# Performance work log

Hardware: AMD Instinct MI355X
Metric: run time of the kernel (lower is better)

Reference implementation:

```python
import jax, jax.numpy as jnp
import numpy as np

SMOOTH = 1.0
MAX_DIST = 10


def _neighbor_conv(x):
    # 3x3 ones kernel with zero center, padding=1 (NCHW, C=1)
    k = jnp.ones((1, 1, 3, 3), x.dtype).at[0, 0, 1, 1].set(0.0)
    return jax.lax.conv_general_dilated(
        x, k, window_strides=(1, 1), padding=[(1, 1), (1, 1)],
        dimension_numbers=('NCHW', 'OIHW', 'NCHW'))


def _analyze_skeleton(skel):
    n = _neighbor_conv(skel)
    on = skel > 0.5
    endpoints = ((n == 1) & on).astype(skel.dtype)
    midpoints = ((n == 2) & on).astype(skel.dtype)
    junctions = ((n > 2) & on).astype(skel.dtype)
    return endpoints, midpoints, junctions


def _iou(p, g):
    inter = jnp.sum(p * g, axis=(2, 3))
    union = jnp.sum(p, axis=(2, 3)) + jnp.sum(g, axis=(2, 3)) - inter
    return (inter + SMOOTH) / (union + SMOOTH)


def _structural_similarity(pred_skel, gt_skel):
    pe, pm, pj = _analyze_skeleton(pred_skel)
    ge, gm, gj = _analyze_skeleton(gt_skel)
    e_iou, m_iou, j_iou = _iou(pe, ge), _iou(pm, gm), _iou(pj, gj)
    ge_c = jnp.sum(ge, axis=(2, 3))
    gj_c = jnp.sum(gj, axis=(2, 3))
    gm_c = jnp.sum(gm, axis=(2, 3))
    total = ge_c + gj_c + gm_c + SMOOTH
    loss = 1.0 - ((ge_c / total) * e_iou + (gj_c / total) * j_iou + (gm_c / total) * m_iou)
    return loss.mean()


def _maxpool3(x):
    return jax.lax.reduce_window(
        x, -jnp.inf, jax.lax.max,
        window_dimensions=(1, 1, 3, 3), window_strides=(1, 1, 1, 1),
        padding=[(0, 0), (0, 0), (1, 1), (1, 1)])


def _distance_approximation(target, reference):
    # Fixed MAX_DIST iterations; identical math to the torch early-exit loop
    # because new_points requires ~found_mask (no distance is overwritten).
    tgt_on = target > 0.5

    def step(carry, d):
        dilated, found, dist = carry
        dilated = _maxpool3(dilated)
        new = (dilated > 0.5) & tgt_on & (~found)
        dist = dist + d.astype(dist.dtype) * new.astype(dist.dtype)
        return (dilated, found | new, dist), None

    init = (reference, jnp.zeros(target.shape, bool), jnp.zeros_like(target))
    (_, found, dist), _ = jax.lax.scan(step, init, jnp.arange(1, MAX_DIST + 1, dtype=jnp.int32))
    unfound = tgt_on & (~found)
    dist = dist + jnp.asarray(MAX_DIST, dist.dtype) * unfound.astype(dist.dtype)
    total_points = jnp.sum(tgt_on.astype(dist.dtype), axis=(2, 3))
    return jnp.sum(dist, axis=(2, 3)) / (total_points + SMOOTH)


def _medial_axis_distance(pred_skel, gt_skel):
    p2g = _distance_approximation(pred_skel, gt_skel)
    g2p = _distance_approximation(gt_skel, pred_skel)
    return (((p2g + g2p) / 2.0) / MAX_DIST).mean()


def setup_inputs() -> dict:
    key = jax.random.key(0)
    k1, k2 = jax.random.split(key)
    B, C, H, W = 32, 1, 512, 512
    pred_skel = jax.random.uniform(k1, (B, C, H, W), dtype=jnp.float32)
    gt_skel = (jax.random.uniform(k2, (B, C, H, W), dtype=jnp.float32) < 0.1).astype(jnp.float32)
    return {"pred_skel": pred_skel, "gt_skel": gt_skel}


def reference(pred_skel, gt_skel):
    inter = jnp.sum(pred_skel * gt_skel, axis=(2, 3))
    psum = jnp.sum(pred_skel, axis=(2, 3))
    gsum = jnp.sum(gt_skel, axis=(2, 3))
    dice = (2.0 * inter + SMOOTH) / (psum + gsum + SMOOTH)
    dice_loss = 1.0 - dice.mean()
    structural_loss = _structural_similarity(pred_skel, gt_skel)
    medial_loss = _medial_axis_distance(pred_skel, gt_skel)
    avg_mag = (dice_loss + structural_loss + medial_loss) / 3.0
    bal_dice = dice_loss / (dice_loss + SMOOTH) * avg_mag
    bal_struct = structural_loss / (structural_loss + SMOOTH) * avg_mag
    bal_medial = medial_loss / (medial_loss + SMOOTH) * avg_mag
    return bal_dice + bal_struct + bal_medial
```

## Files before the change

### kernel.cpp

```cpp
#include <hip/hip_runtime.h>
#include <stdint.h>

#define BATCH 32
#define H 512
#define W 512
#define NACC 16
#define TH 32
#define HALO 9
#define RH (TH + 2*HALO)
#define NWORDS (RH*8)
#define NT 1024
#define NW (NT/64)
#define NTILE (H/TH)
#define NBLK (NTILE*BATCH)


__global__ __launch_bounds__(NT, 4) void fused_kernel(
    const float* __restrict__ pred, const float* __restrict__ gt,
    float* __restrict__ part)
{
    __shared__ uint64_t MpS[NWORDS + 2];
    __shared__ uint64_t MgS[NWORDS + 2];
    __shared__ uint64_t Ge[TH * 8];
    __shared__ uint64_t Gm[TH * 8];
    __shared__ uint64_t Gj[TH * 8];
    __shared__ float    EC[2][TH];
    __shared__ float    redf[NW][2];
    __shared__ unsigned redu[NW][3];

    uint64_t* Mp = MpS + 1;
    uint64_t* Mg = MgS + 1;

    int fid  = blockIdx.x;
    int b    = fid & 31;
    int tile = fid >> 5;

    const float* pimg = pred + (size_t)b * H * W;
    const float* gimg = gt   + (size_t)b * H * W;
    int y0 = tile * TH;
    int tid = threadIdx.x, lane = tid & 63, wid = tid >> 6;

    float v0 = 0.f, v1 = 0.f;
    for (int s0 = wid; s0 < NWORDS; s0 += 4 * NW) {
        float vp[4], vg[4];
        #pragma unroll
        for (int u = 0; u < 4; ++u) {
            int s = s0 + u * NW;
            vp[u] = 0.f; vg[u] = 0.f;
            int ry = y0 - HALO + (s >> 3);
            if (s < NWORDS && (unsigned)ry < (unsigned)H) {
                int i0 = ry * W + (s & 7) * 64 + lane;
                vp[u] = pimg[i0]; vg[u] = gimg[i0];
            }
        }
        #pragma unroll
        for (int u = 0; u < 4; ++u) {
            int s = s0 + u * NW;
            if (s < NWORDS) {
                unsigned long long mp = __ballot(vp[u] > 0.5f);
                unsigned long long mg = __ballot(vg[u] > 0.5f);
                if (lane == 0) { Mp[s] = mp; Mg[s] = mg; }
                int r = s >> 3;
                if (r >= HALO && r < HALO + TH) {
                    v1 += vp[u];
                    v0 += (vg[u] > 0.5f) ? vp[u] : 0.f;
                }
            }
        }
    }
    if (tid == 0) { MpS[0] = 0; MpS[NWORDS + 1] = 0; MgS[0] = 0; MgS[NWORDS + 1] = 0; }

    bool isStencil = tid >= 512;
    int idx = tid & 511;
    int qi = idx & 127, h2 = idx >> 7;
    int x4 = qi * 4;
    int ys = y0 + h2 * 8;
    float4 pm4 = make_float4(0, 0, 0, 0), pc4 = make_float4(0, 0, 0, 0);
    if (isStencil) {
        if (ys > 0) pm4 = *(const float4*)(pimg + (size_t)(ys - 1) * W + x4);
        pc4 = *(const float4*)(pimg + (size_t)ys * W + x4);
    }

    if (tid < 2 * TH) {
        int c = tid >> 5, r = tid & (TH - 1);
        int y = y0 + r, col = 255 + c;
        float sum = (y > 0     ? pimg[(size_t)(y - 1) * W + col] : 0.f)
                  +              pimg[(size_t)y * W + col]
                  + (y < H - 1 ? pimg[(size_t)(y + 1) * W + col] : 0.f);
        EC[c][r] = sum;
    }
    __syncthreads();

    unsigned cge = 0, cgm = 0, cgj = 0;
    if (tid < 256) {
        int r = tid >> 3, w = tid & 7;
        int oM = (HALO + r) * 8 + w;
        bool wl = (w > 0), wr = (w < 7);
        uint64_t A  = Mg[oM - 8], Bm = Mg[oM], Cm = Mg[oM + 8];
        uint64_t AL = wl ? Mg[oM - 9] : 0ULL, AR = wr ? Mg[oM - 7] : 0ULL;
        uint64_t BL = wl ? Mg[oM - 1] : 0ULL, BR = wr ? Mg[oM + 1] : 0ULL;
        uint64_t CL = wl ? Mg[oM + 7] : 0ULL, CR = wr ? Mg[oM + 9] : 0ULL;
        uint64_t Aw = (A  << 1) | (AL >> 63), Ae = (A  >> 1) | (AR << 63);
        uint64_t Bw = (Bm << 1) | (BL >> 63), Be = (Bm >> 1) | (BR << 63);
        uint64_t Cw = (Cm << 1) | (CL >> 63), Ce = (Cm >> 1) | (CR << 63);
        uint64_t c1, c2, c3, c5;
        uint64_t t;
        t = Aw ^ A;  uint64_t s1 = t ^ Ae;  c1 = (Aw & A)  | (Ae & t);
        t = Bw ^ Be; uint64_t s2 = t ^ Cw;  c2 = (Bw & Be) | (Cw & t);
        t = Cm ^ Ce; uint64_t s3 = t ^ s1;  c3 = (Cm & Ce) | (s1 & t);
        uint64_t b0 = s2 ^ s3, c4 = s2 & s3;
        t = c1 ^ c2; uint64_t s5 = t ^ c3;  c5 = (c1 & c2) | (c3 & t);
        uint64_t b1 = s5 ^ c4, c6 = s5 & c4;
        uint64_t b2 = c5 ^ c6, b3 = c5 & c6;
        uint64_t nz23 = ~(b2 | b3);
        uint64_t ge = Bm & b0 & ~b1 & nz23;
        uint64_t gm = Bm & b1 & ~b0 & nz23;
        uint64_t gj = Bm & (b2 | b3 | (b1 & b0));
        Ge[tid] = ge; Gm[tid] = gm; Gj[tid] = gj;
        cge = (unsigned)__popcll(ge);
        cgm = (unsigned)__popcll(gm);
        cgj = (unsigned)__popcll(gj);
    }
    __syncthreads();

    uint64_t cpack = 0ULL;
    int dsum = 0, dcnt = 0;

    if (isStencil) {
        int wdx = qi >> 4;
        int ss = (qi & 15) * 4;

        for (int r = 0; r < 8; ++r) {
            int y = ys + r;
            float4 pp4 = (y < H - 1) ? *(const float4*)(pimg + (size_t)(y + 1) * W + x4)
                                     : make_float4(0, 0, 0, 0);
            int ry = h2 * 8 + r;
            uint64_t gew = Ge[ry * 8 + wdx];
            uint64_t gmw = Gm[ry * 8 + wdx];
            uint64_t gjw = Gj[ry * 8 + wdx];

            float ps[6];
            ps[1] = pm4.x + pc4.x + pp4.x; ps[2] = pm4.y + pc4.y + pp4.y;
            ps[3] = pm4.z + pc4.z + pp4.z; ps[4] = pm4.w + pc4.w + pp4.w;
            float psl = __shfl_up(ps[4], 1, 64);
            float psr = __shfl_down(ps[1], 1, 64);
            if (lane == 0)  psl = (qi == 0)   ? 0.f : EC[0][ry];
            if (lane == 63) psr = (qi == 127) ? 0.f : EC[1][ry];
            ps[0] = psl; ps[5] = psr;

            float pcv[4] = {pc4.x, pc4.y, pc4.z, pc4.w};
            #pragma unroll
            for (int j = 0; j < 4; ++j) {
                float np = ps[j] + ps[j + 1] + ps[j + 2] - pcv[j];
                bool pon = pcv[j] > 0.5f;
                bool pe  = pon && (np == 1.f);
                bool pmb = pon && (np == 2.f);
                bool pjb = pon && (np > 2.f);
                unsigned geb = (unsigned)(gew >> (ss + j)) & 1u;
                unsigned gmb = (unsigned)(gmw >> (ss + j)) & 1u;
                unsigned gjb = (unsigned)(gjw >> (ss + j)) & 1u;
                cpack += (uint64_t)pe
                       | ((uint64_t)pmb << 7)
                       | ((uint64_t)pjb << 14)
                       | ((uint64_t)(pe  && geb) << 21)
                       | ((uint64_t)(pmb && gmb) << 28)
                       | ((uint64_t)(pjb && gjb) << 35);
            }
            pm4 = pc4; pc4 = pp4;
        }
    } else {
        bool isP = tid < 256;
        int di = tid & 255;
        int o  = (HALO + (di >> 3)) * 8 + (di & 7);
        int w  = di & 7;
        bool wL = (w > 0), wR = (w < 7);
        const uint64_t* MT = isP ? Mp : Mg;
        const uint64_t* MV = isP ? Mg : Mp;

        uint64_t T = MT[o];
        dcnt = __popcll(T);
        dsum = dcnt;
        uint64_t VM = MV[o];
        uint64_t VL = wL ? MV[o - 1] : 0ULL;
        uint64_t VR = wR ? MV[o + 1] : 0ULL;
        uint64_t C = VM;

        #pragma unroll
        for (int a = 1; a <= 9; ++a) {
            int lo = o - 8 * a, hi = o + 8 * a;
            uint64_t NM = MV[lo] | MV[hi];
            uint64_t NL = wL ? (MV[lo - 1] | MV[hi - 1]) : 0ULL;
            uint64_t NR = wR ? (MV[lo + 1] | MV[hi + 1]) : 0ULL;
            uint64_t SL = NL, SM = NM, SR = NR;
            const int m = a - 1;
            if (m >= 1) {
                SM |= (SM << 1) | (SM >> 1) | (SL >> 63) | (SR << 63);
                SL |= SL << 1; SR |= SR >> 1;
            }
            if (m >= 2) {
                const int s = (m == 2) ? 1 : 2;
                SM |= (SM << s) | (SM >> s) | (SL >> (64 - s)) | (SR << (64 - s));
                SL |= SL << s; SR |= SR >> s;
            }
            if (m >= 4) {
                const int s = (m - 3 < 4) ? (m - 3) : 4;
                SM |= (SM << s) | (SM >> s) | (SL >> (64 - s)) | (SR << (64 - s));
                SL |= SL << s; SR |= SR >> s;
            }
            if (m >= 8) {
                const int s = m - 7;
                SM |= (SM << s) | (SM >> s) | (SL >> (64 - s)) | (SR << (64 - s));
                SL |= SL << s; SR |= SR >> s;
            }
            C |= SM;
            VL |= NL; VM |= NM; VR |= NR;
            C |= (VM << a) | (VM >> a) | (VL >> (64 - a)) | (VR << (64 - a));
            uint64_t rem = T & ~C;
            dsum += __popcll(rem);
            if (__all(rem == 0ULL)) break;
        }
    }

    unsigned r0, r1, r2;
    if (isStencil) {
        unsigned c_pe = (unsigned)( cpack        & 0x7F);
        unsigned c_pm = (unsigned)((cpack >> 7 ) & 0x7F);
        unsigned c_pj = (unsigned)((cpack >> 14) & 0x7F);
        unsigned c_ie = (unsigned)((cpack >> 21) & 0x7F);
        unsigned c_im = (unsigned)((cpack >> 28) & 0x7F);
        unsigned c_ij = (unsigned)((cpack >> 35) & 0x7F);
        r0 = c_pe | (c_pm << 16); r1 = c_pj | (c_ie << 16); r2 = c_im | (c_ij << 16);
    } else {
        r0 = (unsigned)dsum | ((unsigned)dcnt << 16);
        r1 = cge | (cgm << 16);
        r2 = cgj;
    }
    #pragma unroll
    for (int off = 32; off; off >>= 1) {
        v0 += __shfl_down(v0, off, 64);
        v1 += __shfl_down(v1, off, 64);
        r0 += __shfl_down(r0, off, 64);
        r1 += __shfl_down(r1, off, 64);
        r2 += __shfl_down(r2, off, 64);
    }
    if (lane == 0) {
        redf[wid][0] = v0; redf[wid][1] = v1;
        redu[wid][0] = r0; redu[wid][1] = r1; redu[wid][2] = r2;
    }
    __syncthreads();
    if (tid < 16) {
        int k = tid;
        float s = 0.f;
        if (k < 2) {
            #pragma unroll
            for (int wv = 0; wv < NW; ++wv) s += redf[wv][k];
        } else {
            static const uint8_t WB[16] = {0,0, 4, 8,8,8, 0,0,0, 8,8,8, 0,0,4,4};
            static const uint8_t WC[16] = {0,0, 4, 8,8,8, 4,4,4, 8,8,8, 4,4,4,4};
            static const uint8_t RG[16] = {0,0, 0, 0,0,1, 1,1,2, 1,2,2, 0,0,0,0};
            static const uint8_t HI[16] = {0,0, 1, 0,1,0, 0,1,0, 1,0,1, 0,1,0,1};
            unsigned u = 0;
            for (int wv = WB[k]; wv < WB[k] + WC[k]; ++wv)
                u += (redu[wv][RG[k]] >> (HI[k] * 16)) & 0xFFFFu;
            s = (float)u;
        }
        part[fid * NACC + k] = s;
    }
}

__global__ __launch_bounds__(512) void final_kernel(
    const float* __restrict__ part, float* __restrict__ out)
{
    __shared__ float sacc[BATCH][NACC];
    __shared__ float tri[BATCH][3];
    int t = threadIdx.x;
    {
        int b = t >> 4, k = t & 15;
        float s = 0.f;
        #pragma unroll 4
        for (int j = 0; j < NTILE; ++j)
            s += part[((j << 5) + b) * NACC + k];
        sacc[b][k] = s;
    }
    __syncthreads();
    if (t < BATCH) {
        const float* a = sacc[t];
        float inter = a[0], psum = a[1], gsum = a[2];
        float dice = (2.f * inter + 1.f) / (psum + gsum + 1.f);

        float pe = a[3], pm = a[4], pj = a[5];
        float ge = a[6], gm = a[7], gj = a[8];
        float ie = a[9], im = a[10], ij = a[11];
        float e_iou = (ie + 1.f) / (pe + ge - ie + 1.f);
        float m_iou = (im + 1.f) / (pm + gm - im + 1.f);
        float j_iou = (ij + 1.f) / (pj + gj - ij + 1.f);
        float total = ge + gj + gm + 1.f;
        float sloss = 1.f - ((ge / total) * e_iou + (gj / total) * j_iou + (gm / total) * m_iou);

        float p2g = a[12] / (a[13] + 1.f);
        float g2p = a[14] / (a[15] + 1.f);
        float med = ((p2g + g2p) * 0.5f) / 10.f;
        tri[t][0] = dice; tri[t][1] = sloss; tri[t][2] = med;
    }
    __syncthreads();
    if (t == 0) {
        float dice = 0.f, sloss = 0.f, med = 0.f;
        for (int b = 0; b < BATCH; ++b) {
            dice += tri[b][0]; sloss += tri[b][1]; med += tri[b][2];
        }
        float dice_loss  = 1.f - dice / (float)BATCH;
        float structural = sloss / (float)BATCH;
        float medial     = med / (float)BATCH;
        float avg = (dice_loss + structural + medial) / 3.f;
        float r = dice_loss  / (dice_loss  + 1.f) * avg
                + structural / (structural + 1.f) * avg
                + medial     / (medial     + 1.f) * avg;
        out[0] = r;
    }
}

extern "C" void kernel_launch(void* const* d_in, const int* in_sizes, int n_in,
                              void* d_out, int out_size, void* d_ws, size_t ws_size,
                              hipStream_t stream)
{
    const float* pred = (const float*)d_in[0];
    const float* gt   = (const float*)d_in[1];
    float* part = (float*)d_ws;
    float* out  = (float*)d_out;

    fused_kernel<<<dim3(NBLK), NT, 0, stream>>>(pred, gt, part);
    final_kernel<<<1, 512, 0, stream>>>(part, out);
}
```

Baseline: 112.0 us.

## Spread stencil and distance search across all threads with 32-bit words

The old kernel split work by thread role: 512 threads ran the float stencil over 8 rows each while 512 ran the distance search on 64-bit mask words. Now all 1024 threads run the stencil over 4 rows each, and all 1024 run the distance search on 32-bit half-words, which halves per-thread shift/popcount width. The aim is to balance the two phases and remove idle divergence between role groups. In exchange the reduction needs more shuffle channels and a reworked lookup table, and the 32-bit search uses twice as many neighbour-word loads.

```diff
diff --git a/kernel.cpp b/kernel.cpp
--- a/kernel.cpp
+++ b/kernel.cpp
@@ -26,7 +26,7 @@
     __shared__ uint64_t Gj[TH * 8];
     __shared__ float    EC[2][TH];
     __shared__ float    redf[NW][2];
-    __shared__ unsigned redu[NW][3];
+    __shared__ unsigned redu[NW][6];
 
     uint64_t* Mp = MpS + 1;
     uint64_t* Mg = MgS + 1;
@@ -70,16 +70,12 @@
     }
     if (tid == 0) { MpS[0] = 0; MpS[NWORDS + 1] = 0; MgS[0] = 0; MgS[NWORDS + 1] = 0; }
 
-    bool isStencil = tid >= 512;
-    int idx = tid & 511;
-    int qi = idx & 127, h2 = idx >> 7;
+    int qi = tid & 127, band = tid >> 7;
     int x4 = qi * 4;
-    int ys = y0 + h2 * 8;
-    float4 pm4 = make_float4(0, 0, 0, 0), pc4 = make_float4(0, 0, 0, 0);
-    if (isStencil) {
-        if (ys > 0) pm4 = *(const float4*)(pimg + (size_t)(ys - 1) * W + x4);
-        pc4 = *(const float4*)(pimg + (size_t)ys * W + x4);
-    }
+    int ys = y0 + band * 4;
+    float4 pm4 = make_float4(0, 0, 0, 0), pc4;
+    if (ys > 0) pm4 = *(const float4*)(pimg + (size_t)(ys - 1) * W + x4);
+    pc4 = *(const float4*)(pimg + (size_t)ys * W + x4);
 
     if (tid < 2 * TH) {
         int c = tid >> 5, r = tid & (TH - 1);
@@ -103,8 +99,7 @@
         uint64_t Aw = (A  << 1) | (AL >> 63), Ae = (A  >> 1) | (AR << 63);
         uint64_t Bw = (Bm << 1) | (BL >> 63), Be = (Bm >> 1) | (BR << 63);
         uint64_t Cw = (Cm << 1) | (CL >> 63), Ce = (Cm >> 1) | (CR << 63);
-        uint64_t c1, c2, c3, c5;
-        uint64_t t;
+        uint64_t c1, c2, c3, c5, t;
         t = Aw ^ A;  uint64_t s1 = t ^ Ae;  c1 = (Aw & A)  | (Ae & t);
         t = Bw ^ Be; uint64_t s2 = t ^ Cw;  c2 = (Bw & Be) | (Cw & t);
         t = Cm ^ Ce; uint64_t s3 = t ^ s1;  c3 = (Cm & Ce) | (s1 & t);
@@ -121,20 +116,73 @@
         cgm = (unsigned)__popcll(gm);
         cgj = (unsigned)__popcll(gj);
     }
+
+    int dsum = 0, dcnt = 0;
+    {
+        const uint32_t* Mp32 = (const uint32_t*)Mp;
+        const uint32_t* Mg32 = (const uint32_t*)Mg;
+        bool isP = tid < 512;
+        int di = tid & 511;
+        int o  = (HALO + (di >> 4)) * 16 + (di & 15);
+        int h  = di & 15;
+        bool wL = (h > 0), wR = (h < 15);
+        const uint32_t* MT = isP ? Mp32 : Mg32;
+        const uint32_t* MV = isP ? Mg32 : Mp32;
+
+        uint32_t T = MT[o];
+        dcnt = __popc(T);
+        dsum = dcnt;
+        uint32_t VM = MV[o];
+        uint32_t VL = wL ? MV[o - 1] : 0u;
+        uint32_t VR = wR ? MV[o + 1] : 0u;
+        uint32_t C = VM;
+
+        #pragma unroll
+        for (int a = 1; a <= 9; ++a) {
+            int lo = o - 16 * a, hi = o + 16 * a;
+            uint32_t NM = MV[lo] | MV[hi];
+            uint32_t NL = wL ? (MV[lo - 1] | MV[hi - 1]) : 0u;
+            uint32_t NR = wR ? (MV[lo + 1] | MV[hi + 1]) : 0u;
+            uint32_t SL = NL, SM = NM, SR = NR;
+            const int m = a - 1;
+            if (m >= 1) {
+                SM |= (SM << 1) | (SM >> 1) | (SL >> 31) | (SR << 31);
+                SL |= SL << 1; SR |= SR >> 1;
+            }
+            if (m >= 2) {
+                const int s = (m == 2) ? 1 : 2;
+                SM |= (SM << s) | (SM >> s) | (SL >> (32 - s)) | (SR << (32 - s));
+                SL |= SL << s; SR |= SR >> s;
+            }
+            if (m >= 4) {
+                const int s = (m - 3 < 4) ? (m - 3) : 4;
+                SM |= (SM << s) | (SM >> s) | (SL >> (32 - s)) | (SR << (32 - s));
+                SL |= SL << s; SR |= SR >> s;
+            }
+            if (m >= 8) {
+                const int s = m - 7;
+                SM |= (SM << s) | (SM >> s) | (SL >> (32 - s)) | (SR << (32 - s));
+                SL |= SL << s; SR |= SR >> s;
+            }
+            C |= SM;
+            VL |= NL; VM |= NM; VR |= NR;
+            C |= (VM << a) | (VM >> a) | (VL >> (32 - a)) | (VR << (32 - a));
+            uint32_t rem = T & ~C;
+            dsum += __popc(rem);
+            if (__all(rem == 0u)) break;
+        }
+    }
     __syncthreads();
 
     uint64_t cpack = 0ULL;
-    int dsum = 0, dcnt = 0;
-
-    if (isStencil) {
+    {
         int wdx = qi >> 4;
         int ss = (qi & 15) * 4;
-
-        for (int r = 0; r < 8; ++r) {
+        for (int r = 0; r < 4; ++r) {
             int y = ys + r;
             float4 pp4 = (y < H - 1) ? *(const float4*)(pimg + (size_t)(y + 1) * W + x4)
                                      : make_float4(0, 0, 0, 0);
-            int ry = h2 * 8 + r;
+            int ry = band * 4 + r;
             uint64_t gew = Ge[ry * 8 + wdx];
             uint64_t gmw = Gm[ry * 8 + wdx];
             uint64_t gjw = Gj[ry * 8 + wdx];
@@ -168,73 +216,20 @@
             }
             pm4 = pc4; pc4 = pp4;
         }
-    } else {
-        bool isP = tid < 256;
-        int di = tid & 255;
-        int o  = (HALO + (di >> 3)) * 8 + (di & 7);
-        int w  = di & 7;
-        bool wL = (w > 0), wR = (w < 7);
-        const uint64_t* MT = isP ? Mp : Mg;
-        const uint64_t* MV = isP ? Mg : Mp;
-
-        uint64_t T = MT[o];
-        dcnt = __popcll(T);
-        dsum = dcnt;
-        uint64_t VM = MV[o];
-        uint64_t VL = wL ? MV[o - 1] : 0ULL;
-        uint64_t VR = wR ? MV[o + 1] : 0ULL;
-        uint64_t C = VM;
-
-        #pragma unroll
-        for (int a = 1; a <= 9; ++a) {
-            int lo = o - 8 * a, hi = o + 8 * a;
-            uint64_t NM = MV[lo] | MV[hi];
-            uint64_t NL = wL ? (MV[lo - 1] | MV[hi - 1]) : 0ULL;
-            uint64_t NR = wR ? (MV[lo + 1] | MV[hi + 1]) : 0ULL;
-            uint64_t SL = NL, SM = NM, SR = NR;
-            const int m = a - 1;
-            if (m >= 1) {
-                SM |= (SM << 1) | (SM >> 1) | (SL >> 63) | (SR << 63);
-                SL |= SL << 1; SR |= SR >> 1;
-            }
-            if (m >= 2) {
-                const int s = (m == 2) ? 1 : 2;
-                SM |= (SM << s) | (SM >> s) | (SL >> (64 - s)) | (SR << (64 - s));
-                SL |= SL << s; SR |= SR >> s;
-            }
-            if (m >= 4) {
-                const int s = (m - 3 < 4) ? (m - 3) : 4;
-                SM |= (SM << s) | (SM >> s) | (SL >> (64 - s)) | (SR << (64 - s));
-                SL |= SL << s; SR |= SR >> s;
-            }
-            if (m >= 8) {
-                const int s = m - 7;
-                SM |= (SM << s) | (SM >> s) | (SL >> (64 - s)) | (SR << (64 - s));
-                SL |= SL << s; SR |= SR >> s;
-            }
-            C |= SM;
-            VL |= NL; VM |= NM; VR |= NR;
-            C |= (VM << a) | (VM >> a) | (VL >> (64 - a)) | (VR << (64 - a));
-            uint64_t rem = T & ~C;
-            dsum += __popcll(rem);
-            if (__all(rem == 0ULL)) break;
-        }
-    }
-
-    unsigned r0, r1, r2;
-    if (isStencil) {
-        unsigned c_pe = (unsigned)( cpack        & 0x7F);
-        unsigned c_pm = (unsigned)((cpack >> 7 ) & 0x7F);
-        unsigned c_pj = (unsigned)((cpack >> 14) & 0x7F);
-        unsigned c_ie = (unsigned)((cpack >> 21) & 0x7F);
-        unsigned c_im = (unsigned)((cpack >> 28) & 0x7F);
-        unsigned c_ij = (unsigned)((cpack >> 35) & 0x7F);
-        r0 = c_pe | (c_pm << 16); r1 = c_pj | (c_ie << 16); r2 = c_im | (c_ij << 16);
-    } else {
-        r0 = (unsigned)dsum | ((unsigned)dcnt << 16);
-        r1 = cge | (cgm << 16);
-        r2 = cgj;
-    }
+    }
+
+    unsigned c_pe = (unsigned)( cpack        & 0x7F);
+    unsigned c_pm = (unsigned)((cpack >> 7 ) & 0x7F);
+    unsigned c_pj = (unsigned)((cpack >> 14) & 0x7F);
+    unsigned c_ie = (unsigned)((cpack >> 21) & 0x7F);
+    unsigned c_im = (unsigned)((cpack >> 28) & 0x7F);
+    unsigned c_ij = (unsigned)((cpack >> 35) & 0x7F);
+    unsigned r0 = (unsigned)dsum | ((unsigned)dcnt << 16);
+    unsigned r1 = c_pe | (c_pm << 16);
+    unsigned r2 = c_pj | (c_ie << 16);
+    unsigned r3 = c_im | (c_ij << 16);
+    unsigned r4 = cge | (cgm << 16);
+    unsigned r5 = cgj;
     #pragma unroll
     for (int off = 32; off; off >>= 1) {
         v0 += __shfl_down(v0, off, 64);
@@ -242,10 +237,14 @@
         r0 += __shfl_down(r0, off, 64);
         r1 += __shfl_down(r1, off, 64);
         r2 += __shfl_down(r2, off, 64);
+        r3 += __shfl_down(r3, off, 64);
+        r4 += __shfl_down(r4, off, 64);
+        r5 += __shfl_down(r5, off, 64);
     }
     if (lane == 0) {
         redf[wid][0] = v0; redf[wid][1] = v1;
         redu[wid][0] = r0; redu[wid][1] = r1; redu[wid][2] = r2;
+        redu[wid][3] = r3; redu[wid][4] = r4; redu[wid][5] = r5;
     }
     __syncthreads();
     if (tid < 16) {
@@ -255,10 +254,10 @@
             #pragma unroll
             for (int wv = 0; wv < NW; ++wv) s += redf[wv][k];
         } else {
-            static const uint8_t WB[16] = {0,0, 4, 8,8,8, 0,0,0, 8,8,8, 0,0,4,4};
-            static const uint8_t WC[16] = {0,0, 4, 8,8,8, 4,4,4, 8,8,8, 4,4,4,4};
-            static const uint8_t RG[16] = {0,0, 0, 0,0,1, 1,1,2, 1,2,2, 0,0,0,0};
-            static const uint8_t HI[16] = {0,0, 1, 0,1,0, 0,1,0, 1,0,1, 0,1,0,1};
+            static const uint8_t WB[16] = {0,0, 8, 0,0,0,  0,0,0, 0,0,0,   0,0,8,8};
+            static const uint8_t WC[16] = {0,0, 8, 16,16,16, 4,4,4, 16,16,16, 8,8,8,8};
+            static const uint8_t RG[16] = {0,0, 0, 1,1,2,  4,4,5, 2,3,3,   0,0,0,0};
+            static const uint8_t HI[16] = {0,0, 1, 0,1,0,  0,1,0, 1,0,1,   0,1,0,1};
             unsigned u = 0;
             for (int wv = WB[k]; wv < WB[k] + WC[k]; ++wv)
                 u += (redu[wv][RG[k]] >> (HI[k] * 16)) & 0xFFFFu;
```

Result: no change. 111.6 us (-0.4%).

## Halve block size and run distance and stencil phases sequentially per thread

Applied to the files above, without the earlier changes.

The block shrinks from 1024 to 512 threads. Instead of splitting the threads into separate stencil and distance-search groups, every thread now runs the bitmask distance search and then the 8-row stencil pass. The reduction carries six packed counters and two float accumulator pairs, and the lookup tables are remapped to match. This targets idle time from the imbalance between the two groups and may allow more resident blocks, but it lengthens each thread's serial path and raises register pressure.

```diff
diff --git a/kernel.cpp b/kernel.cpp
--- a/kernel.cpp
+++ b/kernel.cpp
@@ -9,8 +9,8 @@
 #define HALO 9
 #define RH (TH + 2*HALO)
 #define NWORDS (RH*8)
-#define NT 1024
-#define NW (NT/64)
+#define NT 512
+#define NW 8
 #define NTILE (H/TH)
 #define NBLK (NTILE*BATCH)
 
@@ -25,8 +25,8 @@
     __shared__ uint64_t Gm[TH * 8];
     __shared__ uint64_t Gj[TH * 8];
     __shared__ float    EC[2][TH];
-    __shared__ float    redf[NW][2];
-    __shared__ unsigned redu[NW][3];
+    __shared__ float    redf[16][2];
+    __shared__ unsigned redu[NW][6];
 
     uint64_t* Mp = MpS + 1;
     uint64_t* Mg = MgS + 1;
@@ -40,7 +40,7 @@
     int y0 = tile * TH;
     int tid = threadIdx.x, lane = tid & 63, wid = tid >> 6;
 
-    float v0 = 0.f, v1 = 0.f;
+    float v0A = 0.f, v1A = 0.f, v0B = 0.f, v1B = 0.f;
     for (int s0 = wid; s0 < NWORDS; s0 += 4 * NW) {
         float vp[4], vg[4];
         #pragma unroll
@@ -62,24 +62,25 @@
                 if (lane == 0) { Mp[s] = mp; Mg[s] = mg; }
                 int r = s >> 3;
                 if (r >= HALO && r < HALO + TH) {
-                    v1 += vp[u];
-                    v0 += (vg[u] > 0.5f) ? vp[u] : 0.f;
+                    if ((u & 1) == 0) {
+                        v1A += vp[u];
+                        v0A += (vg[u] > 0.5f) ? vp[u] : 0.f;
+                    } else {
+                        v1B += vp[u];
+                        v0B += (vg[u] > 0.5f) ? vp[u] : 0.f;
+                    }
                 }
             }
         }
     }
     if (tid == 0) { MpS[0] = 0; MpS[NWORDS + 1] = 0; MgS[0] = 0; MgS[NWORDS + 1] = 0; }
 
-    bool isStencil = tid >= 512;
-    int idx = tid & 511;
-    int qi = idx & 127, h2 = idx >> 7;
+    int qi = tid & 127, h2 = tid >> 7;
     int x4 = qi * 4;
     int ys = y0 + h2 * 8;
-    float4 pm4 = make_float4(0, 0, 0, 0), pc4 = make_float4(0, 0, 0, 0);
-    if (isStencil) {
-        if (ys > 0) pm4 = *(const float4*)(pimg + (size_t)(ys - 1) * W + x4);
-        pc4 = *(const float4*)(pimg + (size_t)ys * W + x4);
-    }
+    float4 pm4 = make_float4(0, 0, 0, 0), pc4;
+    if (ys > 0) pm4 = *(const float4*)(pimg + (size_t)(ys - 1) * W + x4);
+    pc4 = *(const float4*)(pimg + (size_t)ys * W + x4);
 
     if (tid < 2 * TH) {
         int c = tid >> 5, r = tid & (TH - 1);
@@ -93,8 +94,8 @@
 
     unsigned cge = 0, cgm = 0, cgj = 0;
     if (tid < 256) {
-        int r = tid >> 3, w = tid & 7;
-        int oM = (HALO + r) * 8 + w;
+        int rr = tid >> 3, w = tid & 7;
+        int oM = (HALO + rr) * 8 + w;
         bool wl = (w > 0), wr = (w < 7);
         uint64_t A  = Mg[oM - 8], Bm = Mg[oM], Cm = Mg[oM + 8];
         uint64_t AL = wl ? Mg[oM - 9] : 0ULL, AR = wr ? Mg[oM - 7] : 0ULL;
@@ -103,8 +104,7 @@
         uint64_t Aw = (A  << 1) | (AL >> 63), Ae = (A  >> 1) | (AR << 63);
         uint64_t Bw = (Bm << 1) | (BL >> 63), Be = (Bm >> 1) | (BR << 63);
         uint64_t Cw = (Cm << 1) | (CL >> 63), Ce = (Cm >> 1) | (CR << 63);
-        uint64_t c1, c2, c3, c5;
-        uint64_t t;
+        uint64_t c1, c2, c3, c5, t;
         t = Aw ^ A;  uint64_t s1 = t ^ Ae;  c1 = (Aw & A)  | (Ae & t);
         t = Bw ^ Be; uint64_t s2 = t ^ Cw;  c2 = (Bw & Be) | (Cw & t);
         t = Cm ^ Ce; uint64_t s3 = t ^ s1;  c3 = (Cm & Ce) | (s1 & t);
@@ -121,15 +121,66 @@
         cgm = (unsigned)__popcll(gm);
         cgj = (unsigned)__popcll(gj);
     }
+
+    int dsum = 0, dcnt = 0;
+    {
+        bool isP = tid < 256;
+        int di = tid & 255;
+        int o  = (HALO + (di >> 3)) * 8 + (di & 7);
+        int w  = di & 7;
+        bool wL = (w > 0), wR = (w < 7);
+        const uint64_t* MT = isP ? Mp : Mg;
+        const uint64_t* MV = isP ? Mg : Mp;
+
+        uint64_t T = MT[o];
+        dcnt = __popcll(T);
+        dsum = dcnt;
+        uint64_t VM = MV[o];
+        uint64_t VL = wL ? MV[o - 1] : 0ULL;
+        uint64_t VR = wR ? MV[o + 1] : 0ULL;
+        uint64_t C = VM;
+
+        #pragma unroll
+        for (int a = 1; a <= 9; ++a) {
+            int lo = o - 8 * a, hi = o + 8 * a;
+            uint64_t NM = MV[lo] | MV[hi];
+            uint64_t NL = wL ? (MV[lo - 1] | MV[hi - 1]) : 0ULL;
+            uint64_t NR = wR ? (MV[lo + 1] | MV[hi + 1]) : 0ULL;
+            uint64_t SL = NL, SM = NM, SR = NR;
+            const int m = a - 1;
+            if (m >= 1) {
+                SM |= (SM << 1) | (SM >> 1) | (SL >> 63) | (SR << 63);
+                SL |= SL << 1; SR |= SR >> 1;
+            }
+            if (m >= 2) {
+                const int s = (m == 2) ? 1 : 2;
+                SM |= (SM << s) | (SM >> s) | (SL >> (64 - s)) | (SR << (64 - s));
+                SL |= SL << s; SR |= SR >> s;
+            }
+            if (m >= 4) {
+                const int s = (m - 3 < 4) ? (m - 3) : 4;
+                SM |= (SM << s) | (SM >> s) | (SL >> (64 - s)) | (SR << (64 - s));
+                SL |= SL << s; SR |= SR >> s;
+            }
+            if (m >= 8) {
+                const int s = m - 7;
+                SM |= (SM << s) | (SM >> s) | (SL >> (64 - s)) | (SR << (64 - s));
+                SL |= SL << s; SR |= SR >> s;
+            }
+            C |= SM;
+            VL |= NL; VM |= NM; VR |= NR;
+            C |= (VM << a) | (VM >> a) | (VL >> (64 - a)) | (VR << (64 - a));
+            uint64_t rem = T & ~C;
+            dsum += __popcll(rem);
+            if (__all(rem == 0ULL)) break;
+        }
+    }
     __syncthreads();
 
     uint64_t cpack = 0ULL;
-    int dsum = 0, dcnt = 0;
-
-    if (isStencil) {
+    {
         int wdx = qi >> 4;
         int ss = (qi & 15) * 4;
-
         for (int r = 0; r < 8; ++r) {
             int y = ys + r;
             float4 pp4 = (y < H - 1) ? *(const float4*)(pimg + (size_t)(y + 1) * W + x4)
@@ -168,84 +219,38 @@
             }
             pm4 = pc4; pc4 = pp4;
         }
-    } else {
-        bool isP = tid < 256;
-        int di = tid & 255;
-        int o  = (HALO + (di >> 3)) * 8 + (di & 7);
-        int w  = di & 7;
-        bool wL = (w > 0), wR = (w < 7);
-        const uint64_t* MT = isP ? Mp : Mg;
-        const uint64_t* MV = isP ? Mg : Mp;
-
-        uint64_t T = MT[o];
-        dcnt = __popcll(T);
-        dsum = dcnt;
-        uint64_t VM = MV[o];
-        uint64_t VL = wL ? MV[o - 1] : 0ULL;
-        uint64_t VR = wR ? MV[o + 1] : 0ULL;
-        uint64_t C = VM;
-
-        #pragma unroll
-        for (int a = 1; a <= 9; ++a) {
-            int lo = o - 8 * a, hi = o + 8 * a;
-            uint64_t NM = MV[lo] | MV[hi];
-            uint64_t NL = wL ? (MV[lo - 1] | MV[hi - 1]) : 0ULL;
-            uint64_t NR = wR ? (MV[lo + 1] | MV[hi + 1]) : 0ULL;
-            uint64_t SL = NL, SM = NM, SR = NR;
-            const int m = a - 1;
-            if (m >= 1) {
-                SM |= (SM << 1) | (SM >> 1) | (SL >> 63) | (SR << 63);
-                SL |= SL << 1; SR |= SR >> 1;
-            }
-            if (m >= 2) {
-                const int s = (m == 2) ? 1 : 2;
-                SM |= (SM << s) | (SM >> s) | (SL >> (64 - s)) | (SR << (64 - s));
-                SL |= SL << s; SR |= SR >> s;
-            }
-            if (m >= 4) {
-                const int s = (m - 3 < 4) ? (m - 3) : 4;
-                SM |= (SM << s) | (SM >> s) | (SL >> (64 - s)) | (SR << (64 - s));
-                SL |= SL << s; SR |= SR >> s;
-            }
-            if (m >= 8) {
-                const int s = m - 7;
-                SM |= (SM << s) | (SM >> s) | (SL >> (64 - s)) | (SR << (64 - s));
-                SL |= SL << s; SR |= SR >> s;
-            }
-            C |= SM;
-            VL |= NL; VM |= NM; VR |= NR;
-            C |= (VM << a) | (VM >> a) | (VL >> (64 - a)) | (VR << (64 - a));
-            uint64_t rem = T & ~C;
-            dsum += __popcll(rem);
-            if (__all(rem == 0ULL)) break;
-        }
-    }
-
-    unsigned r0, r1, r2;
-    if (isStencil) {
-        unsigned c_pe = (unsigned)( cpack        & 0x7F);
-        unsigned c_pm = (unsigned)((cpack >> 7 ) & 0x7F);
-        unsigned c_pj = (unsigned)((cpack >> 14) & 0x7F);
-        unsigned c_ie = (unsigned)((cpack >> 21) & 0x7F);
-        unsigned c_im = (unsigned)((cpack >> 28) & 0x7F);
-        unsigned c_ij = (unsigned)((cpack >> 35) & 0x7F);
-        r0 = c_pe | (c_pm << 16); r1 = c_pj | (c_ie << 16); r2 = c_im | (c_ij << 16);
-    } else {
-        r0 = (unsigned)dsum | ((unsigned)dcnt << 16);
-        r1 = cge | (cgm << 16);
-        r2 = cgj;
-    }
+    }
+
+    unsigned c_pe = (unsigned)( cpack        & 0x7F);
+    unsigned c_pm = (unsigned)((cpack >> 7 ) & 0x7F);
+    unsigned c_pj = (unsigned)((cpack >> 14) & 0x7F);
+    unsigned c_ie = (unsigned)((cpack >> 21) & 0x7F);
+    unsigned c_im = (unsigned)((cpack >> 28) & 0x7F);
+    unsigned c_ij = (unsigned)((cpack >> 35) & 0x7F);
+    unsigned r0 = (unsigned)dsum | ((unsigned)dcnt << 16);
+    unsigned r1 = c_pe | (c_pm << 16);
+    unsigned r2 = c_pj | (c_ie << 16);
+    unsigned r3 = c_im | (c_ij << 16);
+    unsigned r4 = cge | (cgm << 16);
+    unsigned r5 = cgj;
     #pragma unroll
     for (int off = 32; off; off >>= 1) {
-        v0 += __shfl_down(v0, off, 64);
-        v1 += __shfl_down(v1, off, 64);
+        v0A += __shfl_down(v0A, off, 64);
+        v1A += __shfl_down(v1A, off, 64);
+        v0B += __shfl_down(v0B, off, 64);
+        v1B += __shfl_down(v1B, off, 64);
         r0 += __shfl_down(r0, off, 64);
         r1 += __shfl_down(r1, off, 64);
         r2 += __shfl_down(r2, off, 64);
+        r3 += __shfl_down(r3, off, 64);
+        r4 += __shfl_down(r4, off, 64);
+        r5 += __shfl_down(r5, off, 64);
     }
     if (lane == 0) {
-        redf[wid][0] = v0; redf[wid][1] = v1;
+        redf[wid][0] = v0A;     redf[wid][1] = v1A;
+        redf[wid + 8][0] = v0B; redf[wid + 8][1] = v1B;
         redu[wid][0] = r0; redu[wid][1] = r1; redu[wid][2] = r2;
+        redu[wid][3] = r3; redu[wid][4] = r4; redu[wid][5] = r5;
     }
     __syncthreads();
     if (tid < 16) {
@@ -253,11 +258,11 @@
         float s = 0.f;
         if (k < 2) {
             #pragma unroll
-            for (int wv = 0; wv < NW; ++wv) s += redf[wv][k];
+            for (int wv = 0; wv < 16; ++wv) s += redf[wv][k];
         } else {
-            static const uint8_t WB[16] = {0,0, 4, 8,8,8, 0,0,0, 8,8,8, 0,0,4,4};
+            static const uint8_t WB[16] = {0,0, 4, 0,0,0, 0,0,0, 0,0,0, 0,0,4,4};
             static const uint8_t WC[16] = {0,0, 4, 8,8,8, 4,4,4, 8,8,8, 4,4,4,4};
-            static const uint8_t RG[16] = {0,0, 0, 0,0,1, 1,1,2, 1,2,2, 0,0,0,0};
+            static const uint8_t RG[16] = {0,0, 0, 1,1,2, 4,4,5, 2,3,3, 0,0,0,0};
             static const uint8_t HI[16] = {0,0, 1, 0,1,0, 0,1,0, 1,0,1, 0,1,0,1};
             unsigned u = 0;
             for (int wv = WB[k]; wv < WB[k] + WC[k]; ++wv)
```

New measurement: 113.1 us. No clear change (+1.0%).
